# Optimization experiments

Hardware: AMD Instinct MI355X
Metric: run time of the kernel (lower is better)

The kernel has to match this reference:

```python
import jax, jax.numpy as jnp
import numpy as np

B, H, T, D = 2, 16, 2048, 64
BASE_WINDOW = 256
FULL = 999999


def _make_window_sizes(num_heads=H, base_window=BASE_WINDOW):
    ws = []
    for h in range(num_heads):
        if h < num_heads // 4:
            ws.append(base_window)
        elif h < num_heads // 2:
            ws.append(base_window * 2)
        elif h < 3 * num_heads // 4:
            ws.append(base_window * 4)
        else:
            ws.append(FULL)
    return jnp.asarray(ws, dtype=jnp.int32)


def setup_inputs() -> dict:
    key = jax.random.key(0)
    kq, kk, kv = jax.random.split(key, 3)
    Q = jax.random.normal(kq, (B, H, T, D), dtype=jnp.float32)
    K = jax.random.normal(kk, (B, H, T, D), dtype=jnp.float32)
    V = jax.random.normal(kv, (B, H, T, D), dtype=jnp.float32)
    return {"Q": Q, "K": K, "V": V, "window_sizes": _make_window_sizes()}


def reference(Q, K, V, window_sizes):
    b, h, t, d = Q.shape
    scale = 1.0 / np.sqrt(d).astype(np.float32)
    idx = jnp.arange(t, dtype=jnp.int32)
    diff = idx[:, None] - idx[None, :]  # [T, T], q_idx - kv_idx
    # causal & |q-k| <= w  ==  0 <= diff <= w  (per head)
    mask = (diff >= 0) & (diff[None, :, :] <= window_sizes[:, None, None])  # [H, T, T]
    scores = jnp.einsum('bhqd,bhkd->bhqk', Q, K) * scale  # [B, H, T, T]
    scores = jnp.where(mask[None], scores, -jnp.inf)
    attn = jax.nn.softmax(scores, axis=-1)
    return jnp.einsum('bhqk,bhkd->bhqd', attn, V)
```

## Files before the change

kernel.cpp:

```cpp
#include <hip/hip_runtime.h>
#include <hip/hip_bf16.h>


constexpr int Bc = 2, Hc = 16, Tc = 2048, Dc = 64;
constexpr int BQ = 64;
constexpr int BK = 64;
constexpr int KSTR = 72;
constexpr int VSTR = 72;
constexpr int PSTR = 72;
constexpr int N_ITEMS = Bc * Hc * (Tc / BQ);
constexpr float QSCALE = 0.125f * 1.44269504088896340736f;
constexpr float CMAX = 16.0f;

constexpr size_t KB_OFF = 256;
constexpr size_t VB_OFF = 256 + (size_t)Bc * Hc * Tc * Dc * 2;
constexpr int HEADE = Tc * Dc;

constexpr int KOFF = 0;
constexpr int VOFF = 9216;
constexpr int POFF = 20736;
constexpr int IBOFF = 29952;

typedef __attribute__((ext_vector_type(8))) short short8;
typedef __attribute__((ext_vector_type(4))) float float4v;

__device__ inline unsigned f2bf_u(float f) {
    union { float f; unsigned u; } v; v.f = f;
    return (v.u + 0x7fffu + ((v.u >> 16) & 1u)) >> 16;
}

__device__ inline short8 pack8(const float* t) {
    short8 r;
#pragma unroll
    for (int j = 0; j < 8; j++) r[j] = (short)f2bf_u(t[j]);
    return r;
}

__device__ inline unsigned pk_bf16(float a, float b) {
    __hip_bfloat162 h = __float22bfloat162_rn(make_float2(a, b));
    union { __hip_bfloat162 h; unsigned u; } v; v.h = h;
    return v.u;
}

__global__ __launch_bounds__(256)
void preconv_kernel(const float* __restrict__ K, const float* __restrict__ V,
                    unsigned short* __restrict__ Kb, unsigned short* __restrict__ Vtb) {
    const int blk = blockIdx.x;
    const int tid = threadIdx.x;
    if (blk < 2048) {
        const int base = blk * 2048 + tid * 8;
        float4v a = *(const float4v*)(K + base);
        float4v b = *(const float4v*)(K + base + 4);
        float t[8] = {a[0], a[1], a[2], a[3], b[0], b[1], b[2], b[3]};
        *(short8*)(Kb + base) = pack8(t);
    } else {
        __shared__ float tile[64][65];
        const int blk2 = blk - 2048;
        const int bh = blk2 >> 5;
        const int t0 = (blk2 & 31) * 64;
        const float* src = V + (size_t)bh * HEADE + (size_t)t0 * Dc;
#pragma unroll
        for (int i = 0; i < 4; i++) {
            const int r = (tid >> 4) + i * 16;
            const int d4 = (tid & 15) * 4;
            float4v v4 = *(const float4v*)(src + r * Dc + d4);
            tile[r][d4] = v4[0]; tile[r][d4 + 1] = v4[1];
            tile[r][d4 + 2] = v4[2]; tile[r][d4 + 3] = v4[3];
        }
        __syncthreads();
        unsigned short* dst = Vtb + (size_t)bh * HEADE + t0;
#pragma unroll
        for (int i = 0; i < 2; i++) {
            const int d = (tid >> 3) + 32 * i;
            const int c = tid & 7;
            float t[8];
#pragma unroll
            for (int j = 0; j < 8; j++) t[j] = tile[c * 8 + j][d];
            *(short8*)(dst + (size_t)d * Tc + c * 8) = pack8(t);
        }
    }
}

__global__ __launch_bounds__(512, 4)
void dswa_kernel(const float* __restrict__ Q,
                 const unsigned short* __restrict__ Kb,
                 const unsigned short* __restrict__ Vtb,
                 const int* __restrict__ wsz,
                 float* __restrict__ O, unsigned* __restrict__ counter) {
    __shared__ __align__(16) unsigned short LDS[29960];

    const int tid  = threadIdx.x;
    const int g    = tid >> 8;
    const int ltid = tid & 255;
    const int wave = tid >> 6;
    const int wv   = wave & 3;
    const int lane = tid & 63;
    const int quad = lane >> 4;
    const int l16  = lane & 15;

    unsigned short* Kl = &LDS[KOFF + g * 4608];
    unsigned short* Vt = &LDS[VOFF + g * 5760];
    unsigned short* Pl = &LDS[POFF + wave * 1152];
    int* ib = (int*)&LDS[IBOFF];

    for (int i = ltid; i < 16 * VSTR; i += 256) {
        const int row = i / VSTR, col = i % VSTR;
        Vt[(64 + row) * VSTR + col] = (row == 0 && col < 64) ? 0x3F80 : 0;
    }

    const int srow = ltid >> 3;
    const int scol = (ltid & 7) * 8;

    for (;;) {
        if (tid == 0) *ib = (int)atomicAdd(counter, 1u);
        __syncthreads();
        const int idx = *ib;
        if (idx >= N_ITEMS) break;

        const int b  = idx & 1;
        const int qt = 31 - ((idx >> 1) & 31);
        const int h  = 15 - (idx >> 6);
        const int q0 = qt * BQ;
        const int win = wsz[h];

        const size_t headoff = (size_t)(b * Hc + h) * HEADE;
        const float* Qp = Q + headoff;
        const unsigned short* Kbh = Kb + headoff;
        const unsigned short* Vbh = Vtb + headoff;
        float* Op = O + headoff;

        short8 qf[2];
        {
            const int qrow = q0 + wv * 16 + l16;
#pragma unroll
            for (int c = 0; c < 2; c++) {
                const float* src = Qp + (size_t)qrow * Dc + c * 32 + quad * 8;
                float4v a = *(const float4v*)src;
                float4v d4 = *(const float4v*)(src + 4);
                float t[8] = {a[0]*QSCALE, a[1]*QSCALE, a[2]*QSCALE, a[3]*QSCALE,
                              d4[0]*QSCALE, d4[1]*QSCALE, d4[2]*QSCALE, d4[3]*QSCALE};
                qf[c] = pack8(t);
            }
        }

        float4v acc[4];
        float4v acc5;
#pragma unroll
        for (int nb = 0; nb < 4; nb++) acc[nb] = (float4v){0.f, 0.f, 0.f, 0.f};
        acc5 = (float4v){0.f, 0.f, 0.f, 0.f};

        const int kv_lo = (max(0, q0 - win)) & ~(BK - 1);
        const int n_tiles = (q0 + BQ - kv_lo) >> 6;
        const int IT = (n_tiles + 1) >> 1;

        const int rw0 = q0 + wv * 16;
        const int rg_rel0 = rw0 + l16 - quad * 4;

        short8 kr0, kr1, vr0, vr1;
        if (g < n_tiles) {
            const int kv0 = kv_lo + g * BK;
            kr0 = *(const short8*)(Kbh + (size_t)(kv0 + srow) * Dc + scol);
            kr1 = *(const short8*)(Kbh + (size_t)(kv0 + srow + 32) * Dc + scol);
            vr0 = *(const short8*)(Vbh + (size_t)srow * Tc + kv0 + scol);
            vr1 = *(const short8*)(Vbh + (size_t)(srow + 32) * Tc + kv0 + scol);
        }

        for (int t = 0; t < IT; ++t) {
            const int ti = g + 2 * t;
            const bool act = ti < n_tiles;
            const int kv0 = kv_lo + ti * BK;

            __syncthreads();

            if (act) {
                *(short8*)&Kl[srow * KSTR + scol] = kr0;
                *(short8*)&Kl[(srow + 32) * KSTR + scol] = kr1;
                *(short8*)&Vt[srow * VSTR + scol] = vr0;
                *(short8*)&Vt[(srow + 32) * VSTR + scol] = vr1;
            }
            __syncthreads();

            const int tn = ti + 2;
            if (tn < n_tiles) {
                const int kvn = kv_lo + tn * BK;
                kr0 = *(const short8*)(Kbh + (size_t)(kvn + srow) * Dc + scol);
                kr1 = *(const short8*)(Kbh + (size_t)(kvn + srow + 32) * Dc + scol);
                vr0 = *(const short8*)(Vbh + (size_t)srow * Tc + kvn + scol);
                vr1 = *(const short8*)(Vbh + (size_t)(srow + 32) * Tc + kvn + scol);
            }

            if (act) {
                float4v sT[4];
#pragma unroll
                for (int mb = 0; mb < 4; mb++) {
                    float4v c = {-CMAX, -CMAX, -CMAX, -CMAX};
#pragma unroll
                    for (int ch = 0; ch < 2; ch++) {
                        short8 kf = *(short8*)&Kl[(mb * 16 + l16) * KSTR + ch * 32 + quad * 8];
                        c = __builtin_amdgcn_mfma_f32_16x16x32_bf16(kf, qf[ch], c, 0, 0, 0);
                    }
                    sT[mb] = c;
                }

                const bool interior = (rw0 >= kv0 + 63) && (rw0 + 15 - kv0 <= win);
                if (!interior) {
                    const int dbase = rg_rel0 - kv0;
#pragma unroll
                    for (int mb = 0; mb < 4; mb++)
#pragma unroll
                        for (int r = 0; r < 4; r++) {
                            const unsigned diff = (unsigned)(dbase - mb * 16 - r);
                            sT[mb][r] = (diff <= (unsigned)win) ? sT[mb][r] : -3.0e38f;
                        }
                }

                float p[4][4];
#pragma unroll
                for (int mb = 0; mb < 4; mb++)
#pragma unroll
                    for (int r = 0; r < 4; r++)
                        p[mb][r] = exp2f(sT[mb][r]);

#pragma unroll
                for (int mb = 0; mb < 4; mb++) {
                    unsigned* dst = (unsigned*)&Pl[l16 * PSTR + mb * 16 + quad * 4];
                    dst[0] = pk_bf16(p[mb][0], p[mb][1]);
                    dst[1] = pk_bf16(p[mb][2], p[mb][3]);
                }

                __asm__ volatile("" ::: "memory");
                short8 pf[2];
#pragma unroll
                for (int ch = 0; ch < 2; ch++)
                    pf[ch] = *(short8*)&Pl[l16 * PSTR + ch * 32 + quad * 8];
#pragma unroll
                for (int nb = 0; nb < 4; nb++) {
#pragma unroll
                    for (int ch = 0; ch < 2; ch++) {
                        short8 vf = *(short8*)&Vt[(nb * 16 + l16) * VSTR + ch * 32 + quad * 8];
                        acc[nb] = __builtin_amdgcn_mfma_f32_16x16x32_bf16(pf[ch], vf, acc[nb], 0, 0, 0);
                    }
                }
#pragma unroll
                for (int ch = 0; ch < 2; ch++) {
                    short8 vf = *(short8*)&Vt[(64 + l16) * VSTR + ch * 32 + quad * 8];
                    acc5 = __builtin_amdgcn_mfma_f32_16x16x32_bf16(pf[ch], vf, acc5, 0, 0, 0);
                }
            }
        }

        __syncthreads();
        float* fl = (float*)LDS;
        if (g == 1) {
#pragma unroll
            for (int r = 0; r < 4; r++) {
                const int row = wv * 16 + quad * 4 + r;
#pragma unroll
                for (int nb = 0; nb < 4; nb++)
                    fl[row * 66 + nb * 16 + l16] = acc[nb][r];
                if (l16 == 0) fl[row * 66 + 64] = acc5[r];
            }
        }
        __syncthreads();
        if (g == 0) {
#pragma unroll
            for (int r = 0; r < 4; r++) {
                const int row = wv * 16 + quad * 4 + r;
                const float l0 = __shfl(acc5[r], quad * 16);
                const float lt = l0 + fl[row * 66 + 64];
                const float inv = 1.0f / lt;
                float* dst = Op + (size_t)(q0 + row) * Dc;
#pragma unroll
                for (int nb = 0; nb < 4; nb++)
                    dst[nb * 16 + l16] = (acc[nb][r] + fl[row * 66 + nb * 16 + l16]) * inv;
            }
        }
    }
}

extern "C" void kernel_launch(void* const* d_in, const int* in_sizes, int n_in,
                              void* d_out, int out_size, void* d_ws, size_t ws_size,
                              hipStream_t stream) {
    (void)in_sizes; (void)n_in; (void)ws_size; (void)out_size;
    const float* Q = (const float*)d_in[0];
    const float* K = (const float*)d_in[1];
    const float* V = (const float*)d_in[2];
    const int* wsz = (const int*)d_in[3];
    float* Out = (float*)d_out;

    unsigned* counter = (unsigned*)d_ws;
    unsigned short* Kb  = (unsigned short*)((char*)d_ws + KB_OFF);
    unsigned short* Vtb = (unsigned short*)((char*)d_ws + VB_OFF);

    hipMemsetAsync(counter, 0, sizeof(unsigned), stream);
    preconv_kernel<<<dim3(3072), dim3(256), 0, stream>>>(K, V, Kb, Vtb);
    dswa_kernel<<<dim3(512), dim3(512), 0, stream>>>(Q, Kb, Vtb, wsz, Out, counter);
}
```

Baseline: 130.6 us.

## Switch to per-wave 16-row query work items reading K/V directly from global

Restructures the attention kernel so each wave independently grabs a 16-query-row work item via its own atomic counter and loads K and V fragments straight from global memory into registers. This removes the LDS staging of K/V tiles, the block-wide barriers, the split-KV cross-group reduction, and the ones-column MFMA used for the row sum, which is now accumulated in registers with shuffles. It also uses the hardware exp2 builtin. The cost is that K/V reuse across the four waves of a block is lost, so each wave re-reads K/V through cache, raising global and L2 traffic.

```diff
diff --git a/kernel.cpp b/kernel.cpp
--- a/kernel.cpp
+++ b/kernel.cpp
@@ -3,12 +3,9 @@
 
 
 constexpr int Bc = 2, Hc = 16, Tc = 2048, Dc = 64;
-constexpr int BQ = 64;
 constexpr int BK = 64;
-constexpr int KSTR = 72;
-constexpr int VSTR = 72;
 constexpr int PSTR = 72;
-constexpr int N_ITEMS = Bc * Hc * (Tc / BQ);
+constexpr int N_ITEMS = Bc * Hc * (Tc / 16);
 constexpr float QSCALE = 0.125f * 1.44269504088896340736f;
 constexpr float CMAX = 16.0f;
 
@@ -16,13 +13,17 @@
 constexpr size_t VB_OFF = 256 + (size_t)Bc * Hc * Tc * Dc * 2;
 constexpr int HEADE = Tc * Dc;
 
-constexpr int KOFF = 0;
-constexpr int VOFF = 9216;
-constexpr int POFF = 20736;
-constexpr int IBOFF = 29952;
-
 typedef __attribute__((ext_vector_type(8))) short short8;
 typedef __attribute__((ext_vector_type(4))) float float4v;
+
+#if defined(__has_builtin)
+#if __has_builtin(__builtin_amdgcn_exp2f)
+#define EXP2 __builtin_amdgcn_exp2f
+#endif
+#endif
+#ifndef EXP2
+#define EXP2 exp2f
+#endif
 
 __device__ inline unsigned f2bf_u(float f) {
     union { float f; unsigned u; } v; v.f = f;
@@ -81,46 +82,32 @@
     }
 }
 
-__global__ __launch_bounds__(512, 4)
+__global__ __launch_bounds__(256, 4)
 void dswa_kernel(const float* __restrict__ Q,
                  const unsigned short* __restrict__ Kb,
                  const unsigned short* __restrict__ Vtb,
                  const int* __restrict__ wsz,
                  float* __restrict__ O, unsigned* __restrict__ counter) {
-    __shared__ __align__(16) unsigned short LDS[29960];
+    __shared__ __align__(16) unsigned short Pbuf[4 * 16 * PSTR];
 
     const int tid  = threadIdx.x;
-    const int g    = tid >> 8;
-    const int ltid = tid & 255;
     const int wave = tid >> 6;
-    const int wv   = wave & 3;
     const int lane = tid & 63;
     const int quad = lane >> 4;
     const int l16  = lane & 15;
 
-    unsigned short* Kl = &LDS[KOFF + g * 4608];
-    unsigned short* Vt = &LDS[VOFF + g * 5760];
-    unsigned short* Pl = &LDS[POFF + wave * 1152];
-    int* ib = (int*)&LDS[IBOFF];
-
-    for (int i = ltid; i < 16 * VSTR; i += 256) {
-        const int row = i / VSTR, col = i % VSTR;
-        Vt[(64 + row) * VSTR + col] = (row == 0 && col < 64) ? 0x3F80 : 0;
-    }
-
-    const int srow = ltid >> 3;
-    const int scol = (ltid & 7) * 8;
+    unsigned short* Pl = &Pbuf[wave * 16 * PSTR];
 
     for (;;) {
-        if (tid == 0) *ib = (int)atomicAdd(counter, 1u);
-        __syncthreads();
-        const int idx = *ib;
-        if (idx >= N_ITEMS) break;
+        int idx;
+        if (lane == 0) idx = (int)atomicAdd(counter, 1u);
+        idx = __shfl(idx, 0);
+        if (idx >= N_ITEMS) return;
 
         const int b  = idx & 1;
-        const int qt = 31 - ((idx >> 1) & 31);
-        const int h  = 15 - (idx >> 6);
-        const int q0 = qt * BQ;
+        const int qc = 127 - ((idx >> 1) & 127);
+        const int h  = 15 - (idx >> 8);
+        const int q0 = qc * 16;
         const int win = wsz[h];
 
         const size_t headoff = (size_t)(b * Hc + h) * HEADE;
@@ -130,150 +117,98 @@
         float* Op = O + headoff;
 
         short8 qf[2];
-        {
-            const int qrow = q0 + wv * 16 + l16;
-#pragma unroll
-            for (int c = 0; c < 2; c++) {
-                const float* src = Qp + (size_t)qrow * Dc + c * 32 + quad * 8;
-                float4v a = *(const float4v*)src;
-                float4v d4 = *(const float4v*)(src + 4);
-                float t[8] = {a[0]*QSCALE, a[1]*QSCALE, a[2]*QSCALE, a[3]*QSCALE,
-                              d4[0]*QSCALE, d4[1]*QSCALE, d4[2]*QSCALE, d4[3]*QSCALE};
-                qf[c] = pack8(t);
-            }
+#pragma unroll
+        for (int c = 0; c < 2; c++) {
+            const float* src = Qp + (size_t)(q0 + l16) * Dc + c * 32 + quad * 8;
+            float4v a = *(const float4v*)src;
+            float4v d4 = *(const float4v*)(src + 4);
+            float t[8] = {a[0]*QSCALE, a[1]*QSCALE, a[2]*QSCALE, a[3]*QSCALE,
+                          d4[0]*QSCALE, d4[1]*QSCALE, d4[2]*QSCALE, d4[3]*QSCALE};
+            qf[c] = pack8(t);
         }
 
         float4v acc[4];
-        float4v acc5;
 #pragma unroll
         for (int nb = 0; nb < 4; nb++) acc[nb] = (float4v){0.f, 0.f, 0.f, 0.f};
-        acc5 = (float4v){0.f, 0.f, 0.f, 0.f};
+        float lp = 0.0f;
 
         const int kv_lo = (max(0, q0 - win)) & ~(BK - 1);
-        const int n_tiles = (q0 + BQ - kv_lo) >> 6;
-        const int IT = (n_tiles + 1) >> 1;
-
-        const int rw0 = q0 + wv * 16;
-        const int rg_rel0 = rw0 + l16 - quad * 4;
-
-        short8 kr0, kr1, vr0, vr1;
-        if (g < n_tiles) {
-            const int kv0 = kv_lo + g * BK;
-            kr0 = *(const short8*)(Kbh + (size_t)(kv0 + srow) * Dc + scol);
-            kr1 = *(const short8*)(Kbh + (size_t)(kv0 + srow + 32) * Dc + scol);
-            vr0 = *(const short8*)(Vbh + (size_t)srow * Tc + kv0 + scol);
-            vr1 = *(const short8*)(Vbh + (size_t)(srow + 32) * Tc + kv0 + scol);
-        }
-
-        for (int t = 0; t < IT; ++t) {
-            const int ti = g + 2 * t;
-            const bool act = ti < n_tiles;
+        const int n_tiles = ((q0 + 15 - kv_lo) >> 6) + 1;
+
+        for (int ti = 0; ti < n_tiles; ++ti) {
             const int kv0 = kv_lo + ti * BK;
 
-            __syncthreads();
-
-            if (act) {
-                *(short8*)&Kl[srow * KSTR + scol] = kr0;
-                *(short8*)&Kl[(srow + 32) * KSTR + scol] = kr1;
-                *(short8*)&Vt[srow * VSTR + scol] = vr0;
-                *(short8*)&Vt[(srow + 32) * VSTR + scol] = vr1;
-            }
-            __syncthreads();
-
-            const int tn = ti + 2;
-            if (tn < n_tiles) {
-                const int kvn = kv_lo + tn * BK;
-                kr0 = *(const short8*)(Kbh + (size_t)(kvn + srow) * Dc + scol);
-                kr1 = *(const short8*)(Kbh + (size_t)(kvn + srow + 32) * Dc + scol);
-                vr0 = *(const short8*)(Vbh + (size_t)srow * Tc + kvn + scol);
-                vr1 = *(const short8*)(Vbh + (size_t)(srow + 32) * Tc + kvn + scol);
-            }
-
-            if (act) {
-                float4v sT[4];
-#pragma unroll
-                for (int mb = 0; mb < 4; mb++) {
-                    float4v c = {-CMAX, -CMAX, -CMAX, -CMAX};
-#pragma unroll
-                    for (int ch = 0; ch < 2; ch++) {
-                        short8 kf = *(short8*)&Kl[(mb * 16 + l16) * KSTR + ch * 32 + quad * 8];
-                        c = __builtin_amdgcn_mfma_f32_16x16x32_bf16(kf, qf[ch], c, 0, 0, 0);
+            short8 kf[8];
+#pragma unroll
+            for (int mb = 0; mb < 4; mb++)
+#pragma unroll
+                for (int ch = 0; ch < 2; ch++)
+                    kf[mb * 2 + ch] = *(const short8*)
+                        (Kbh + (size_t)(kv0 + mb * 16 + l16) * Dc + ch * 32 + quad * 8);
+
+            float4v sT[4];
+#pragma unroll
+            for (int mb = 0; mb < 4; mb++) {
+                float4v c = {-CMAX, -CMAX, -CMAX, -CMAX};
+                c = __builtin_amdgcn_mfma_f32_16x16x32_bf16(kf[mb * 2 + 0], qf[0], c, 0, 0, 0);
+                c = __builtin_amdgcn_mfma_f32_16x16x32_bf16(kf[mb * 2 + 1], qf[1], c, 0, 0, 0);
+                sT[mb] = c;
+            }
+
+            short8 vf[8];
+#pragma unroll
+            for (int nb = 0; nb < 4; nb++)
+#pragma unroll
+                for (int ch = 0; ch < 2; ch++)
+                    vf[nb * 2 + ch] = *(const short8*)
+                        (Vbh + (size_t)(nb * 16 + l16) * Tc + kv0 + ch * 32 + quad * 8);
+
+            const bool interior = (kv0 + 63 <= q0) && (kv0 >= q0 + 15 - win);
+            if (!interior) {
+                const int dbase = q0 + l16 - kv0 - quad * 4;
+#pragma unroll
+                for (int mb = 0; mb < 4; mb++)
+#pragma unroll
+                    for (int r = 0; r < 4; r++) {
+                        const unsigned diff = (unsigned)(dbase - mb * 16 - r);
+                        sT[mb][r] = (diff <= (unsigned)win) ? sT[mb][r] : -3.0e38f;
                     }
-                    sT[mb] = c;
-                }
-
-                const bool interior = (rw0 >= kv0 + 63) && (rw0 + 15 - kv0 <= win);
-                if (!interior) {
-                    const int dbase = rg_rel0 - kv0;
-#pragma unroll
-                    for (int mb = 0; mb < 4; mb++)
-#pragma unroll
-                        for (int r = 0; r < 4; r++) {
-                            const unsigned diff = (unsigned)(dbase - mb * 16 - r);
-                            sT[mb][r] = (diff <= (unsigned)win) ? sT[mb][r] : -3.0e38f;
-                        }
-                }
-
-                float p[4][4];
-#pragma unroll
-                for (int mb = 0; mb < 4; mb++)
-#pragma unroll
-                    for (int r = 0; r < 4; r++)
-                        p[mb][r] = exp2f(sT[mb][r]);
-
-#pragma unroll
-                for (int mb = 0; mb < 4; mb++) {
-                    unsigned* dst = (unsigned*)&Pl[l16 * PSTR + mb * 16 + quad * 4];
-                    dst[0] = pk_bf16(p[mb][0], p[mb][1]);
-                    dst[1] = pk_bf16(p[mb][2], p[mb][3]);
-                }
-
-                __asm__ volatile("" ::: "memory");
-                short8 pf[2];
-#pragma unroll
-                for (int ch = 0; ch < 2; ch++)
-                    pf[ch] = *(short8*)&Pl[l16 * PSTR + ch * 32 + quad * 8];
-#pragma unroll
-                for (int nb = 0; nb < 4; nb++) {
-#pragma unroll
-                    for (int ch = 0; ch < 2; ch++) {
-                        short8 vf = *(short8*)&Vt[(nb * 16 + l16) * VSTR + ch * 32 + quad * 8];
-                        acc[nb] = __builtin_amdgcn_mfma_f32_16x16x32_bf16(pf[ch], vf, acc[nb], 0, 0, 0);
-                    }
-                }
-#pragma unroll
-                for (int ch = 0; ch < 2; ch++) {
-                    short8 vf = *(short8*)&Vt[(64 + l16) * VSTR + ch * 32 + quad * 8];
-                    acc5 = __builtin_amdgcn_mfma_f32_16x16x32_bf16(pf[ch], vf, acc5, 0, 0, 0);
-                }
-            }
-        }
-
-        __syncthreads();
-        float* fl = (float*)LDS;
-        if (g == 1) {
-#pragma unroll
-            for (int r = 0; r < 4; r++) {
-                const int row = wv * 16 + quad * 4 + r;
-#pragma unroll
-                for (int nb = 0; nb < 4; nb++)
-                    fl[row * 66 + nb * 16 + l16] = acc[nb][r];
-                if (l16 == 0) fl[row * 66 + 64] = acc5[r];
-            }
-        }
-        __syncthreads();
-        if (g == 0) {
-#pragma unroll
-            for (int r = 0; r < 4; r++) {
-                const int row = wv * 16 + quad * 4 + r;
-                const float l0 = __shfl(acc5[r], quad * 16);
-                const float lt = l0 + fl[row * 66 + 64];
-                const float inv = 1.0f / lt;
-                float* dst = Op + (size_t)(q0 + row) * Dc;
-#pragma unroll
-                for (int nb = 0; nb < 4; nb++)
-                    dst[nb * 16 + l16] = (acc[nb][r] + fl[row * 66 + nb * 16 + l16]) * inv;
-            }
+            }
+
+#pragma unroll
+            for (int mb = 0; mb < 4; mb++) {
+                float p0 = EXP2(sT[mb][0]);
+                float p1 = EXP2(sT[mb][1]);
+                float p2 = EXP2(sT[mb][2]);
+                float p3 = EXP2(sT[mb][3]);
+                lp += (p0 + p1) + (p2 + p3);
+                unsigned* dst = (unsigned*)&Pl[l16 * PSTR + mb * 16 + quad * 4];
+                dst[0] = pk_bf16(p0, p1);
+                dst[1] = pk_bf16(p2, p3);
+            }
+
+            __asm__ volatile("" ::: "memory");
+            short8 pf[2];
+#pragma unroll
+            for (int ch = 0; ch < 2; ch++)
+                pf[ch] = *(short8*)&Pl[l16 * PSTR + ch * 32 + quad * 8];
+
+#pragma unroll
+            for (int nb = 0; nb < 4; nb++) {
+                acc[nb] = __builtin_amdgcn_mfma_f32_16x16x32_bf16(pf[0], vf[nb * 2 + 0], acc[nb], 0, 0, 0);
+                acc[nb] = __builtin_amdgcn_mfma_f32_16x16x32_bf16(pf[1], vf[nb * 2 + 1], acc[nb], 0, 0, 0);
+            }
+        }
+
+        lp += __shfl_xor(lp, 16);
+        lp += __shfl_xor(lp, 32);
+#pragma unroll
+        for (int r = 0; r < 4; r++) {
+            const float inv = 1.0f / __shfl(lp, quad * 4 + r);
+            float* dst = Op + (size_t)(q0 + quad * 4 + r) * Dc;
+#pragma unroll
+            for (int nb = 0; nb < 4; nb++)
+                dst[nb * 16 + l16] = acc[nb][r] * inv;
         }
     }
 }
@@ -294,5 +229,5 @@
 
     hipMemsetAsync(counter, 0, sizeof(unsigned), stream);
     preconv_kernel<<<dim3(3072), dim3(256), 0, stream>>>(K, V, Kb, Vtb);
-    dswa_kernel<<<dim3(512), dim3(512), 0, stream>>>(Q, Kb, Vtb, wsz, Out, counter);
-}
+    dswa_kernel<<<dim3(1024), dim3(256), 0, stream>>>(Q, Kb, Vtb, wsz, Out, counter);
+}
```

After: 267.9 us. 105% more time.

## Swizzle LDS tiles, compute softmax denominator in registers, raise occupancy

Applied to the files above, without the earlier changes.

Replaces the padded LDS strides with an XOR-swizzled 64-wide layout for K, V and P. This shrinks shared memory and avoids bank conflicts. The row-sum is now accumulated from the exp values in registers and reduced with shuffles, instead of through an extra MFMA against a ones row in V. LDS use drops, so occupancy is raised to 6 blocks per CU with a 768-block persistent grid, and exp2 uses the hardware builtin. The risk is that the denominator now sums fp32 probabilities while the numerator uses bf16-rounded ones, and that higher occupancy adds register pressure.

```diff
diff --git a/kernel.cpp b/kernel.cpp
--- a/kernel.cpp
+++ b/kernel.cpp
@@ -5,9 +5,6 @@
 constexpr int Bc = 2, Hc = 16, Tc = 2048, Dc = 64;
 constexpr int BQ = 64;
 constexpr int BK = 64;
-constexpr int KSTR = 72;
-constexpr int VSTR = 72;
-constexpr int PSTR = 72;
 constexpr int N_ITEMS = Bc * Hc * (Tc / BQ);
 constexpr float QSCALE = 0.125f * 1.44269504088896340736f;
 constexpr float CMAX = 16.0f;
@@ -17,12 +14,21 @@
 constexpr int HEADE = Tc * Dc;
 
 constexpr int KOFF = 0;
-constexpr int VOFF = 9216;
-constexpr int POFF = 20736;
-constexpr int IBOFF = 29952;
+constexpr int VOFF = 8192;
+constexpr int POFF = 16384;
+constexpr int IBOFF = 24576;
 
 typedef __attribute__((ext_vector_type(8))) short short8;
 typedef __attribute__((ext_vector_type(4))) float float4v;
+
+#if defined(__has_builtin)
+#if __has_builtin(__builtin_amdgcn_exp2f)
+#define EXP2 __builtin_amdgcn_exp2f
+#endif
+#endif
+#ifndef EXP2
+#define EXP2 exp2f
+#endif
 
 __device__ inline unsigned f2bf_u(float f) {
     union { float f; unsigned u; } v; v.f = f;
@@ -40,6 +46,10 @@
     __hip_bfloat162 h = __float22bfloat162_rn(make_float2(a, b));
     union { __hip_bfloat162 h; unsigned u; } v; v.h = h;
     return v.u;
+}
+
+__device__ inline int swz(int row, int col8) {
+    return row * 64 + (col8 ^ ((row & 7) << 3));
 }
 
 __global__ __launch_bounds__(256)
@@ -81,13 +91,13 @@
     }
 }
 
-__global__ __launch_bounds__(512, 4)
+__global__ __launch_bounds__(512, 6)
 void dswa_kernel(const float* __restrict__ Q,
                  const unsigned short* __restrict__ Kb,
                  const unsigned short* __restrict__ Vtb,
                  const int* __restrict__ wsz,
                  float* __restrict__ O, unsigned* __restrict__ counter) {
-    __shared__ __align__(16) unsigned short LDS[29960];
+    __shared__ __align__(16) unsigned short LDS[24576 + 8];
 
     const int tid  = threadIdx.x;
     const int g    = tid >> 8;
@@ -97,16 +107,12 @@
     const int lane = tid & 63;
     const int quad = lane >> 4;
     const int l16  = lane & 15;
-
-    unsigned short* Kl = &LDS[KOFF + g * 4608];
-    unsigned short* Vt = &LDS[VOFF + g * 5760];
-    unsigned short* Pl = &LDS[POFF + wave * 1152];
+    const int sw8  = (l16 & 7) << 3;
+
+    unsigned short* Kl = &LDS[KOFF + g * 4096];
+    unsigned short* Vt = &LDS[VOFF + g * 4096];
+    unsigned short* Pl = &LDS[POFF + wave * 1024];
     int* ib = (int*)&LDS[IBOFF];
-
-    for (int i = ltid; i < 16 * VSTR; i += 256) {
-        const int row = i / VSTR, col = i % VSTR;
-        Vt[(64 + row) * VSTR + col] = (row == 0 && col < 64) ? 0x3F80 : 0;
-    }
 
     const int srow = ltid >> 3;
     const int scol = (ltid & 7) * 8;
@@ -144,10 +150,9 @@
         }
 
         float4v acc[4];
-        float4v acc5;
 #pragma unroll
         for (int nb = 0; nb < 4; nb++) acc[nb] = (float4v){0.f, 0.f, 0.f, 0.f};
-        acc5 = (float4v){0.f, 0.f, 0.f, 0.f};
+        float lp = 0.0f;
 
         const int kv_lo = (max(0, q0 - win)) & ~(BK - 1);
         const int n_tiles = (q0 + BQ - kv_lo) >> 6;
@@ -173,10 +178,10 @@
             __syncthreads();
 
             if (act) {
-                *(short8*)&Kl[srow * KSTR + scol] = kr0;
-                *(short8*)&Kl[(srow + 32) * KSTR + scol] = kr1;
-                *(short8*)&Vt[srow * VSTR + scol] = vr0;
-                *(short8*)&Vt[(srow + 32) * VSTR + scol] = vr1;
+                *(short8*)&Kl[swz(srow, scol)] = kr0;
+                *(short8*)&Kl[swz(srow + 32, scol)] = kr1;
+                *(short8*)&Vt[swz(srow, scol)] = vr0;
+                *(short8*)&Vt[swz(srow + 32, scol)] = vr1;
             }
             __syncthreads();
 
@@ -196,7 +201,8 @@
                     float4v c = {-CMAX, -CMAX, -CMAX, -CMAX};
 #pragma unroll
                     for (int ch = 0; ch < 2; ch++) {
-                        short8 kf = *(short8*)&Kl[(mb * 16 + l16) * KSTR + ch * 32 + quad * 8];
+                        short8 kf = *(short8*)&Kl[(mb * 16 + l16) * 64 +
+                                                  ((ch * 32 + quad * 8) ^ sw8)];
                         c = __builtin_amdgcn_mfma_f32_16x16x32_bf16(kf, qf[ch], c, 0, 0, 0);
                     }
                     sT[mb] = c;
@@ -214,51 +220,50 @@
                         }
                 }
 
-                float p[4][4];
-#pragma unroll
-                for (int mb = 0; mb < 4; mb++)
-#pragma unroll
-                    for (int r = 0; r < 4; r++)
-                        p[mb][r] = exp2f(sT[mb][r]);
-
 #pragma unroll
                 for (int mb = 0; mb < 4; mb++) {
-                    unsigned* dst = (unsigned*)&Pl[l16 * PSTR + mb * 16 + quad * 4];
-                    dst[0] = pk_bf16(p[mb][0], p[mb][1]);
-                    dst[1] = pk_bf16(p[mb][2], p[mb][3]);
+                    float p0 = EXP2(sT[mb][0]);
+                    float p1 = EXP2(sT[mb][1]);
+                    float p2 = EXP2(sT[mb][2]);
+                    float p3 = EXP2(sT[mb][3]);
+                    lp += (p0 + p1) + (p2 + p3);
+                    unsigned* dst = (unsigned*)&Pl[l16 * 64 +
+                                                   ((mb * 16 + quad * 4) ^ sw8)];
+                    dst[0] = pk_bf16(p0, p1);
+                    dst[1] = pk_bf16(p2, p3);
                 }
 
                 __asm__ volatile("" ::: "memory");
                 short8 pf[2];
 #pragma unroll
                 for (int ch = 0; ch < 2; ch++)
-                    pf[ch] = *(short8*)&Pl[l16 * PSTR + ch * 32 + quad * 8];
+                    pf[ch] = *(short8*)&Pl[l16 * 64 + ((ch * 32 + quad * 8) ^ sw8)];
+
 #pragma unroll
                 for (int nb = 0; nb < 4; nb++) {
 #pragma unroll
                     for (int ch = 0; ch < 2; ch++) {
-                        short8 vf = *(short8*)&Vt[(nb * 16 + l16) * VSTR + ch * 32 + quad * 8];
+                        short8 vf = *(short8*)&Vt[(nb * 16 + l16) * 64 +
+                                                  ((ch * 32 + quad * 8) ^ sw8)];
                         acc[nb] = __builtin_amdgcn_mfma_f32_16x16x32_bf16(pf[ch], vf, acc[nb], 0, 0, 0);
                     }
                 }
-#pragma unroll
-                for (int ch = 0; ch < 2; ch++) {
-                    short8 vf = *(short8*)&Vt[(64 + l16) * VSTR + ch * 32 + quad * 8];
-                    acc5 = __builtin_amdgcn_mfma_f32_16x16x32_bf16(pf[ch], vf, acc5, 0, 0, 0);
-                }
-            }
-        }
+            }
+        }
+
+        lp += __shfl_xor(lp, 16);
+        lp += __shfl_xor(lp, 32);
 
         __syncthreads();
         float* fl = (float*)LDS;
         if (g == 1) {
+            if (quad == 0) fl[(wv * 16 + l16) * 66 + 64] = lp;
 #pragma unroll
             for (int r = 0; r < 4; r++) {
                 const int row = wv * 16 + quad * 4 + r;
 #pragma unroll
                 for (int nb = 0; nb < 4; nb++)
                     fl[row * 66 + nb * 16 + l16] = acc[nb][r];
-                if (l16 == 0) fl[row * 66 + 64] = acc5[r];
             }
         }
         __syncthreads();
@@ -266,7 +271,7 @@
 #pragma unroll
             for (int r = 0; r < 4; r++) {
                 const int row = wv * 16 + quad * 4 + r;
-                const float l0 = __shfl(acc5[r], quad * 16);
+                const float l0 = __shfl(lp, quad * 4 + r);
                 const float lt = l0 + fl[row * 66 + 64];
                 const float inv = 1.0f / lt;
                 float* dst = Op + (size_t)(q0 + row) * Dc;
@@ -294,5 +299,5 @@
 
     hipMemsetAsync(counter, 0, sizeof(unsigned), stream);
     preconv_kernel<<<dim3(3072), dim3(256), 0, stream>>>(K, V, Kb, Vtb);
-    dswa_kernel<<<dim3(512), dim3(512), 0, stream>>>(Q, Kb, Vtb, wsz, Out, counter);
-}
+    dswa_kernel<<<dim3(768), dim3(512), 0, stream>>>(Q, Kb, Vtb, wsz, Out, counter);
+}
```

Result: slower. 158.9 us (+21.6%).
